# Performance work log

Hardware: AMD Instinct MI355X
Metric: run time of the kernel (lower is better)

## Reference

```python
import jax, jax.numpy as jnp
import numpy as np

# BinarizeConv2dSDP hyperparameters (from init_kwargs): SDP rank K and output scale.
SCALE = 1.0
K = 2
EPS = 1e-5  # BatchNorm2d default eps


@jax.custom_vjp
def binarize(x):
    # deterministic sign binarization (1-bit)
    return jnp.sign(x)

def _bin_fwd(x):
    return jnp.sign(x), x

def _bin_bwd(x, g):
    # straight-through estimator with hardtanh clipping, as in standard BNN training
    return (g * (jnp.abs(x) <= 1.0).astype(g.dtype),)

binarize.defvjp(_bin_fwd, _bin_bwd)


def conv3x3(x, w, stride=1):
    # x: [N, C, H, W], w: [O, I, 3, 3], padding=1
    return jax.lax.conv_general_dilated(
        x, w,
        window_strides=(stride, stride),
        padding=((1, 1), (1, 1)),
        dimension_numbers=("NCHW", "OIHW", "NCHW"),
    )


def binconv(x, w, stride=1):
    # binarized-input, binarized-weight conv with SDP scale
    return conv3x3(binarize(x), binarize(w), stride) * (SCALE / K)


def batchnorm(x, gamma, beta):
    # training-mode BatchNorm2d over (N, H, W)
    m = jnp.mean(x, axis=(0, 2, 3), keepdims=True)
    v = jnp.var(x, axis=(0, 2, 3), keepdims=True)
    xn = (x - m) * jax.lax.rsqrt(v + EPS)
    return xn * gamma[None, :, None, None] + beta[None, :, None, None]


def setup_inputs() -> dict:
    key = jax.random.key(0)
    k1, k2, k3 = jax.random.split(key, 3)
    N, C, H, W = 32, 256, 56, 56
    x = jax.random.normal(k1, (N, C, H, W), dtype=jnp.float32)
    w1 = jax.random.normal(k2, (C, C, 3, 3), dtype=jnp.float32) * 0.05
    w2 = jax.random.normal(k3, (C, C, 3, 3), dtype=jnp.float32) * 0.05
    g1 = jnp.ones((C,), jnp.float32)
    b1 = jnp.zeros((C,), jnp.float32)
    g2 = jnp.ones((C,), jnp.float32)
    b2 = jnp.zeros((C,), jnp.float32)
    return {"x": x, "w1": w1, "g1": g1, "b1": b1, "w2": w2, "g2": g2, "b2": b2}


def reference(x, w1, g1, b1, w2, g2, b2):
    # out = hardtanh(bn1(conv1(x)))
    out = jnp.clip(batchnorm(binconv(x, w1, 1), g1, b1), -1.0, 1.0)
    # out = bn2(conv2(out)) + shortcut(x)  (identity shortcut: stride=1, in_planes==planes)
    out = batchnorm(binconv(out, w2, 1), g2, b2) + x
    # final hardtanh
    return jnp.clip(out, -1.0, 1.0)
```

## Files before the change

kernel.cpp:

```cpp
#include <hip/hip_runtime.h>
#include <stdint.h>

#define NB    32
#define C     256
#define HH    56
#define WW    56
#define HW    3136
#define P_TOT 100352
#define PW    58
#define PHW   3364
#define NPAD  107648
#define EPSBN 1e-5f

__device__ __forceinline__ uint64_t shflx64(uint64_t v, int m) {
    int lo = __shfl_xor((int)(uint32_t)v, m, 64);
    int hi = __shfl_xor((int)(uint32_t)(v >> 32), m, 64);
    return ((uint64_t)(uint32_t)hi << 32) | (uint32_t)lo;
}
__device__ __forceinline__ uint64_t bt64(uint64_t M, int lane) {
    const uint64_t mk[6] = {0x5555555555555555ULL, 0x3333333333333333ULL,
                            0x0F0F0F0F0F0F0F0FULL, 0x00FF00FF00FF00FFULL,
                            0x0000FFFF0000FFFFULL, 0x00000000FFFFFFFFULL};
#pragma unroll
    for (int k = 0; k < 6; ++k) {
        int s = 1 << k;
        uint64_t mA = mk[k];
        uint64_t v = shflx64(M, s);
        M = (lane & s) ? ((M & ~mA) | ((v & ~mA) >> s))
                       : ((M &  mA) | ((v &  mA) << s));
    }
    return M;
}

__global__ __launch_bounds__(256) void pack_wgt(const float* __restrict__ w1,
                                                const float* __restrict__ w2,
                                                uint64_t* __restrict__ pw1,
                                                uint64_t* __restrict__ pw2,
                                                int* __restrict__ pc1,
                                                int* __restrict__ pc2) {
    int gw = blockIdx.x * 4 + (threadIdx.x >> 6);
    int lane = threadIdx.x & 63;
    int set = gw / 9216;
    int r = gw - set * 9216;
    int wd = r & 3, q = r >> 2;
    int t = q % 9, co = q / 9;
    const float* w = set ? w2 : w1;
    float v = w[(size_t)co * 2304 + (size_t)(wd * 64 + lane) * 9 + t];
    unsigned long long m = __ballot(v >= 0.0f);
    if (lane == 0) {
        uint64_t* pw = set ? pw2 : pw1;
        int* pc = set ? pc2 : pc1;
        pw[(size_t)(wd * 256 + co) * 10 + t] = m;
        pc[(co * 9 + t) * 4 + wd] = (int)__popcll(m);
    }
}

__global__ __launch_bounds__(256) void build_K(const int* __restrict__ pc1,
                                               const int* __restrict__ pc2,
                                               unsigned short* __restrict__ K1,
                                               unsigned short* __restrict__ K2) {
    int tid = blockIdx.x * 256 + threadIdx.x;
    int set = tid / 2304;
    int r = tid - set * 2304;
    int pat = r >> 8, co = r & 255;
    int pv = pat / 3, pq = pat - pv * 3;
    const int* pc = set ? pc2 : pc1;
    int k = 0, corr = 0;
#pragma unroll
    for (int t = 0; t < 9; ++t) {
        int ty = t / 3, tx = t - ty * 3;
        bool inv = (pv == 0 && ty == 0) || (pv == 2 && ty == 2) ||
                   (pq == 0 && tx == 0) || (pq == 2 && tx == 2);
        if (inv) {
            ++k;
            const int* p = pc + (co * 9 + t) * 4;
            corr += p[0] + p[1] + p[2] + p[3];
        }
    }
    unsigned short* K = set ? K2 : K1;
    K[pat * 256 + co] = (unsigned short)(256 * (9 - k) + 2 * corr);
}

__global__ __launch_bounds__(256) void zero_halo(uint64_t* __restrict__ px1,
                                                 uint64_t* __restrict__ px2) {
    int idx = blockIdx.x * 256 + threadIdx.x;
    if (idx >= NPAD) return;
    int pp = idx % PHW;
    int ph = pp / PW, pw_ = pp - ph * PW;
    if (ph == 0 || ph == PW - 1 || pw_ == 0 || pw_ == PW - 1) {
#pragma unroll
        for (int wd = 0; wd < 4; ++wd) {
            px1[(size_t)wd * NPAD + idx] = 0ull;
            px2[(size_t)wd * NPAD + idx] = 0ull;
        }
    }
}

__global__ __launch_bounds__(256) void pack_act(const float* __restrict__ x,
                                                uint64_t* __restrict__ px) {
    int wid = blockIdx.x * 4 + (threadIdx.x >> 6);
    int lane = threadIdx.x & 63;
    int wd = wid & 3;
    int g = wid >> 2;
    int n = g / 49, gi = g - n * 49;
    const float* xp = x + ((size_t)n * C + wd * 64) * HW + gi * 64 + lane;
    uint64_t M = 0;
#pragma unroll
    for (int c = 0; c < 64; ++c) {
        float v = xp[(size_t)c * HW];
        unsigned long long m = __ballot(v >= 0.0f);
        if (lane == c) M = m;
    }
    M = bt64(M, lane);
    int p = gi * 64 + lane;
    int h = p / WW, w = p - h * WW;
    px[(size_t)wd * NPAD + (size_t)n * PHW + (size_t)(h + 1) * PW + (w + 1)] = M;
}

__global__ __launch_bounds__(256, 3) void bconv(const uint64_t* __restrict__ px,
                                                const uint64_t* __restrict__ pw,
                                                const unsigned short* __restrict__ Kt,
                                                short* __restrict__ sout) {
    __shared__ uint64_t lw[2560];
    int co0 = blockIdx.y * 64;
#pragma unroll 1
    for (int i = threadIdx.x; i < 2560; i += 256) {
        int wd = i / 640, j = i - wd * 640;
        lw[i] = pw[(size_t)(wd * 256 + co0) * 10 + j];
    }
    __syncthreads();

    int p = blockIdx.x * 256 + threadIdx.x;
    int n = p / HW, rem = p - n * HW;
    int h = rem / WW, w = rem - h * WW;
    size_t pp = (size_t)n * PHW + (size_t)(h + 1) * PW + (w + 1);

    int acc[64];
#pragma unroll
    for (int c = 0; c < 64; ++c) acc[c] = 0;

#pragma unroll 1
    for (int wd = 0; wd < 4; ++wd) {
        const uint64_t* xb = px + (size_t)wd * NPAD + pp;
        uint64_t x0 = xb[-PW - 1], x1 = xb[-PW], x2 = xb[-PW + 1];
        uint64_t x3 = xb[-1],      x4 = xb[0],   x5 = xb[1];
        uint64_t x6 = xb[PW - 1],  x7 = xb[PW],  x8 = xb[PW + 1];
        const uint64_t* wb = lw + wd * 640;
#pragma unroll
        for (int c = 0; c < 64; ++c) {
            const uint64_t* wq = wb + c * 10;
            int r = acc[c];
            r += __popcll(x0 ^ wq[0]);
            r += __popcll(x1 ^ wq[1]);
            r += __popcll(x2 ^ wq[2]);
            r += __popcll(x3 ^ wq[3]);
            r += __popcll(x4 ^ wq[4]);
            r += __popcll(x5 ^ wq[5]);
            r += __popcll(x6 ^ wq[6]);
            r += __popcll(x7 ^ wq[7]);
            r += __popcll(x8 ^ wq[8]);
            acc[c] = r;
        }
    }

    int pv = (h == 0) ? 0 : ((h == HH - 1) ? 2 : 1);
    int pq = (w == 0) ? 0 : ((w == WW - 1) ? 2 : 1);
    const unsigned short* Kp = Kt + (pv * 3 + pq) * 256 + co0;
    short* op = sout + ((size_t)n * C + co0) * HW + rem;
#pragma unroll
    for (int c = 0; c < 64; ++c)
        op[(size_t)c * HW] = (short)((int)Kp[c] - 2 * acc[c]);
}

__global__ __launch_bounds__(256) void stats(const short* __restrict__ s,
                                             const float* __restrict__ g,
                                             const float* __restrict__ b,
                                             float* __restrict__ A,
                                             float* __restrict__ Bv) {
    int c = blockIdx.x;
    int sum = 0;
    long long sq = 0;
#pragma unroll 4
    for (int k = threadIdx.x; k < 12544; k += 256) {
        int n = k / 392, rr = k - n * 392;
        const int4* p = (const int4*)(s + ((size_t)n * C + c) * HW + rr * 8);
        int4 v = *p;
#pragma unroll
        for (int j = 0; j < 4; ++j) {
            int u = (&v.x)[j];
            int s0 = (int)(short)(u & 0xFFFF);
            int s1 = u >> 16;
            sum += s0 + s1;
            sq += (long long)(s0 * s0 + s1 * s1);
        }
    }
    long long lsum = sum;
#pragma unroll
    for (int off = 32; off; off >>= 1) {
        lsum += __shfl_down(lsum, off, 64);
        sq   += __shfl_down(sq,   off, 64);
    }
    __shared__ long long r0[4], r1[4];
    int lane = threadIdx.x & 63, wv = threadIdx.x >> 6;
    if (lane == 0) { r0[wv] = lsum; r1[wv] = sq; }
    __syncthreads();
    if (threadIdx.x == 0) {
        long long S = r0[0] + r0[1] + r0[2] + r0[3];
        long long Q = r1[0] + r1[1] + r1[2] + r1[3];
        float m  = 0.5f  * (float)S / (float)P_TOT;
        float e2 = 0.25f * (float)Q / (float)P_TOT;
        float var = e2 - m * m;
        float a = g[c] * rsqrtf(var + EPSBN);
        A[c]  = 0.5f * a;
        Bv[c] = b[c] - m * a;
    }
}

__global__ __launch_bounds__(256) void bnpack(const short* __restrict__ s,
                                              const float* __restrict__ A,
                                              const float* __restrict__ Bv,
                                              uint64_t* __restrict__ px) {
    __shared__ float sA[256], sB[256];
    sA[threadIdx.x] = A[threadIdx.x];
    sB[threadIdx.x] = Bv[threadIdx.x];
    __syncthreads();
    int wid = blockIdx.x * 4 + (threadIdx.x >> 6);
    int lane = threadIdx.x & 63;
    int wd = wid & 3;
    int g = wid >> 2;
    int n = g / 49, gi = g - n * 49;
    const short* sp = s + ((size_t)n * C + wd * 64) * HW + gi * 64 + lane;
    uint64_t M = 0;
#pragma unroll
    for (int c = 0; c < 64; ++c) {
        float y = (float)sp[(size_t)c * HW] * sA[wd * 64 + c] + sB[wd * 64 + c];
        unsigned long long m = __ballot(y >= 0.0f);
        if (lane == c) M = m;
    }
    M = bt64(M, lane);
    int p = gi * 64 + lane;
    int h = p / WW, w = p - h * WW;
    px[(size_t)wd * NPAD + (size_t)n * PHW + (size_t)(h + 1) * PW + (w + 1)] = M;
}

__global__ __launch_bounds__(256) void finalize(const short* __restrict__ s,
                                                const float* __restrict__ x,
                                                const float* __restrict__ A,
                                                const float* __restrict__ Bv,
                                                float* __restrict__ out) {
    int i = blockIdx.x * 256 + threadIdx.x;
    int c = (i / 784) & 255;
    short4 sv = ((const short4*)s)[i];
    float4 xv = ((const float4*)x)[i];
    float a = A[c], bb = Bv[c];
    float4 o;
    o.x = fminf(1.0f, fmaxf(-1.0f, (float)sv.x * a + bb + xv.x));
    o.y = fminf(1.0f, fmaxf(-1.0f, (float)sv.y * a + bb + xv.y));
    o.z = fminf(1.0f, fmaxf(-1.0f, (float)sv.z * a + bb + xv.z));
    o.w = fminf(1.0f, fmaxf(-1.0f, (float)sv.w * a + bb + xv.w));
    ((float4*)out)[i] = o;
}

extern "C" void kernel_launch(void* const* d_in, const int* in_sizes, int n_in,
                              void* d_out, int out_size, void* d_ws, size_t ws_size,
                              hipStream_t stream) {
    const float* x  = (const float*)d_in[0];
    const float* w1 = (const float*)d_in[1];
    const float* g1 = (const float*)d_in[2];
    const float* b1 = (const float*)d_in[3];
    const float* w2 = (const float*)d_in[4];
    const float* g2 = (const float*)d_in[5];
    const float* b2 = (const float*)d_in[6];
    float* out = (float*)d_out;

    char* ws = (char*)d_ws;
    uint64_t* pw1 = (uint64_t*)ws;          ws += 4 * 256 * 10 * 8;
    uint64_t* pw2 = (uint64_t*)ws;          ws += 4 * 256 * 10 * 8;
    int* pc1 = (int*)ws;                    ws += 9216 * 4;
    int* pc2 = (int*)ws;                    ws += 9216 * 4;
    unsigned short* K1 = (unsigned short*)ws; ws += 8192;
    unsigned short* K2 = (unsigned short*)ws; ws += 8192;
    float* A1 = (float*)ws;                 ws += 1024;
    float* B1 = (float*)ws;                 ws += 1024;
    float* A2 = (float*)ws;                 ws += 1024;
    float* B2 = (float*)ws;                 ws += 1024;
    uint64_t* px1 = (uint64_t*)ws;          ws += (size_t)4 * NPAD * 8;
    uint64_t* px2 = (uint64_t*)ws;          ws += (size_t)4 * NPAD * 8;
    short* s16 = (short*)ws;

    zero_halo<<<(NPAD + 255) / 256, 256, 0, stream>>>(px1, px2);
    pack_wgt<<<4608, 256, 0, stream>>>(w1, w2, pw1, pw2, pc1, pc2);
    build_K<<<18, 256, 0, stream>>>(pc1, pc2, K1, K2);
    pack_act<<<1568, 256, 0, stream>>>(x, px1);

    bconv<<<dim3(P_TOT / 256, 4), 256, 0, stream>>>(px1, pw1, K1, s16);
    stats<<<C, 256, 0, stream>>>(s16, g1, b1, A1, B1);
    bnpack<<<1568, 256, 0, stream>>>(s16, A1, B1, px2);

    bconv<<<dim3(P_TOT / 256, 4), 256, 0, stream>>>(px2, pw2, K2, s16);
    stats<<<C, 256, 0, stream>>>(s16, g2, b2, A2, B2);

    finalize<<<(P_TOT * C / 4) / 256, 256, 0, stream>>>(s16, x, A2, B2, out);
}
```

Baseline: 566.4 us.

## Restructure binary conv to register-resident activations and channel-major scratch layout

```diff
diff --git a/kernel.cpp b/kernel.cpp
--- a/kernel.cpp
+++ b/kernel.cpp
@@ -11,6 +11,9 @@
 #define PHW   3364
 #define NPAD  107648
 #define EPSBN 1e-5f
+
+#define KEEP9(a) asm volatile("" :: "v"(a[0]), "v"(a[1]), "v"(a[2]), "v"(a[3]), \
+    "v"(a[4]), "v"(a[5]), "v"(a[6]), "v"(a[7]), "v"(a[8]))
 
 __device__ __forceinline__ uint64_t shflx64(uint64_t v, int m) {
     int lo = __shfl_xor((int)(uint32_t)v, m, 64);
@@ -50,7 +53,7 @@
     if (lane == 0) {
         uint64_t* pw = set ? pw2 : pw1;
         int* pc = set ? pc2 : pc1;
-        pw[(size_t)(wd * 256 + co) * 10 + t] = m;
+        pw[(size_t)co * 40 + wd * 9 + t] = m;
         pc[(co * 9 + t) * 4 + wd] = (int)__popcll(m);
     }
 }
@@ -81,23 +84,24 @@
     K[pat * 256 + co] = (unsigned short)(256 * (9 - k) + 2 * corr);
 }
 
-__global__ __launch_bounds__(256) void zero_halo(uint64_t* __restrict__ px1,
-                                                 uint64_t* __restrict__ px2) {
-    int idx = blockIdx.x * 256 + threadIdx.x;
-    if (idx >= NPAD) return;
-    int pp = idx % PHW;
-    int ph = pp / PW, pw_ = pp - ph * PW;
-    if (ph == 0 || ph == PW - 1 || pw_ == 0 || pw_ == PW - 1) {
-#pragma unroll
-        for (int wd = 0; wd < 4; ++wd) {
-            px1[(size_t)wd * NPAD + idx] = 0ull;
-            px2[(size_t)wd * NPAD + idx] = 0ull;
-        }
-    }
-}
-
 __global__ __launch_bounds__(256) void pack_act(const float* __restrict__ x,
-                                                uint64_t* __restrict__ px) {
+                                                uint64_t* __restrict__ px1,
+                                                uint64_t* __restrict__ px2) {
+    if (blockIdx.x >= 1568) {
+        int u = (blockIdx.x - 1568) * 256 + threadIdx.x;
+        if (u >= 29184) return;
+        int wd = u & 3, v = u >> 2;
+        int n = v / 228, cell = v - n * 228;
+        int ph, pw_;
+        if (cell < 58)       { ph = 0;          pw_ = cell; }
+        else if (cell < 116) { ph = 57;         pw_ = cell - 58; }
+        else if (cell < 172) { ph = cell - 115; pw_ = 0; }
+        else                 { ph = cell - 171; pw_ = 57; }
+        size_t idx = (size_t)wd * NPAD + (size_t)n * PHW + (size_t)ph * PW + pw_;
+        px1[idx] = 0ull;
+        px2[idx] = 0ull;
+        return;
+    }
     int wid = blockIdx.x * 4 + (threadIdx.x >> 6);
     int lane = threadIdx.x & 63;
     int wd = wid & 3;
@@ -114,95 +118,87 @@
     M = bt64(M, lane);
     int p = gi * 64 + lane;
     int h = p / WW, w = p - h * WW;
-    px[(size_t)wd * NPAD + (size_t)n * PHW + (size_t)(h + 1) * PW + (w + 1)] = M;
-}
-
-__global__ __launch_bounds__(256, 3) void bconv(const uint64_t* __restrict__ px,
-                                                const uint64_t* __restrict__ pw,
+    px1[(size_t)wd * NPAD + (size_t)n * PHW + (size_t)(h + 1) * PW + (w + 1)] = M;
+}
+
+__global__ __launch_bounds__(256, 2) void bconv(const uint64_t* __restrict__ px,
+                                                const uint64_t* __restrict__ pwt,
                                                 const unsigned short* __restrict__ Kt,
                                                 short* __restrict__ sout) {
-    __shared__ uint64_t lw[2560];
-    int co0 = blockIdx.y * 64;
+    __shared__ unsigned short Kl[2304];
 #pragma unroll 1
-    for (int i = threadIdx.x; i < 2560; i += 256) {
-        int wd = i / 640, j = i - wd * 640;
-        lw[i] = pw[(size_t)(wd * 256 + co0) * 10 + j];
-    }
-    __syncthreads();
+    for (int i = threadIdx.x; i < 2304; i += 256) Kl[i] = Kt[i];
 
     int p = blockIdx.x * 256 + threadIdx.x;
     int n = p / HW, rem = p - n * HW;
     int h = rem / WW, w = rem - h * WW;
-    size_t pp = (size_t)n * PHW + (size_t)(h + 1) * PW + (w + 1);
-
-    int acc[64];
-#pragma unroll
-    for (int c = 0; c < 64; ++c) acc[c] = 0;
-
-#pragma unroll 1
+    size_t base = (size_t)n * PHW + (size_t)(h + 1) * PW + (w + 1);
+
+    uint64_t xt[36];
+#pragma unroll
     for (int wd = 0; wd < 4; ++wd) {
-        const uint64_t* xb = px + (size_t)wd * NPAD + pp;
-        uint64_t x0 = xb[-PW - 1], x1 = xb[-PW], x2 = xb[-PW + 1];
-        uint64_t x3 = xb[-1],      x4 = xb[0],   x5 = xb[1];
-        uint64_t x6 = xb[PW - 1],  x7 = xb[PW],  x8 = xb[PW + 1];
-        const uint64_t* wb = lw + wd * 640;
-#pragma unroll
-        for (int c = 0; c < 64; ++c) {
-            const uint64_t* wq = wb + c * 10;
-            int r = acc[c];
-            r += __popcll(x0 ^ wq[0]);
-            r += __popcll(x1 ^ wq[1]);
-            r += __popcll(x2 ^ wq[2]);
-            r += __popcll(x3 ^ wq[3]);
-            r += __popcll(x4 ^ wq[4]);
-            r += __popcll(x5 ^ wq[5]);
-            r += __popcll(x6 ^ wq[6]);
-            r += __popcll(x7 ^ wq[7]);
-            r += __popcll(x8 ^ wq[8]);
-            acc[c] = r;
-        }
-    }
+        const uint64_t* xb = px + (size_t)wd * NPAD + base;
+        xt[wd * 9 + 0] = xb[-PW - 1]; xt[wd * 9 + 1] = xb[-PW]; xt[wd * 9 + 2] = xb[-PW + 1];
+        xt[wd * 9 + 3] = xb[-1];      xt[wd * 9 + 4] = xb[0];   xt[wd * 9 + 5] = xb[1];
+        xt[wd * 9 + 6] = xb[PW - 1];  xt[wd * 9 + 7] = xb[PW];  xt[wd * 9 + 8] = xb[PW + 1];
+    }
+    __syncthreads();
 
     int pv = (h == 0) ? 0 : ((h == HH - 1) ? 2 : 1);
     int pq = (w == 0) ? 0 : ((w == WW - 1) ? 2 : 1);
-    const unsigned short* Kp = Kt + (pv * 3 + pq) * 256 + co0;
-    short* op = sout + ((size_t)n * C + co0) * HW + rem;
-#pragma unroll
-    for (int c = 0; c < 64; ++c)
-        op[(size_t)c * HW] = (short)((int)Kp[c] - 2 * acc[c]);
-}
-
-__global__ __launch_bounds__(256) void stats(const short* __restrict__ s,
-                                             const float* __restrict__ g,
-                                             const float* __restrict__ b,
-                                             float* __restrict__ A,
-                                             float* __restrict__ Bv) {
+    const unsigned short* Krow = Kl + ((pv * 3 + pq) << 8);
+
+    int co0 = blockIdx.y * 64;
+    short* op = sout + (size_t)co0 * P_TOT + p;
+#pragma unroll 2
+    for (int c = 0; c < 64; ++c) {
+        const uint64_t* wq = pwt + (size_t)(co0 + c) * 40;
+        KEEP9((xt + 0)); KEEP9((xt + 9)); KEEP9((xt + 18)); KEEP9((xt + 27));
+        int a0 = 0, a1 = 0, a2 = 0, a3 = 0;
+#pragma unroll
+        for (int t = 0; t < 9; ++t) {
+            a0 += __popcll(xt[t]      ^ wq[t]);
+            a1 += __popcll(xt[9 + t]  ^ wq[9 + t]);
+            a2 += __popcll(xt[18 + t] ^ wq[18 + t]);
+            a3 += __popcll(xt[27 + t] ^ wq[27 + t]);
+        }
+        int dot = (int)Krow[co0 + c] - 2 * (a0 + a1 + a2 + a3);
+        op[(size_t)c * P_TOT] = (short)dot;
+    }
+}
+
+__global__ __launch_bounds__(256) void statsAB(const short* __restrict__ s,
+                                               const float* __restrict__ g,
+                                               const float* __restrict__ b,
+                                               float* __restrict__ A,
+                                               float* __restrict__ Bv) {
     int c = blockIdx.x;
+    const int4* sp = (const int4*)(s + (size_t)c * P_TOT);
     int sum = 0;
-    long long sq = 0;
+    long long sqq = 0;
 #pragma unroll 4
-    for (int k = threadIdx.x; k < 12544; k += 256) {
-        int n = k / 392, rr = k - n * 392;
-        const int4* p = (const int4*)(s + ((size_t)n * C + c) * HW + rr * 8);
-        int4 v = *p;
+    for (int i = threadIdx.x; i < 12544; i += 256) {
+        int4 v = sp[i];
+        int sq8 = 0;
 #pragma unroll
         for (int j = 0; j < 4; ++j) {
             int u = (&v.x)[j];
             int s0 = (int)(short)(u & 0xFFFF);
             int s1 = u >> 16;
             sum += s0 + s1;
-            sq += (long long)(s0 * s0 + s1 * s1);
+            sq8 += s0 * s0 + s1 * s1;
         }
+        sqq += sq8;
     }
     long long lsum = sum;
 #pragma unroll
     for (int off = 32; off; off >>= 1) {
         lsum += __shfl_down(lsum, off, 64);
-        sq   += __shfl_down(sq,   off, 64);
+        sqq  += __shfl_down(sqq,  off, 64);
     }
     __shared__ long long r0[4], r1[4];
     int lane = threadIdx.x & 63, wv = threadIdx.x >> 6;
-    if (lane == 0) { r0[wv] = lsum; r1[wv] = sq; }
+    if (lane == 0) { r0[wv] = lsum; r1[wv] = sqq; }
     __syncthreads();
     if (threadIdx.x == 0) {
         long long S = r0[0] + r0[1] + r0[2] + r0[3];
@@ -220,26 +216,22 @@
                                               const float* __restrict__ A,
                                               const float* __restrict__ Bv,
                                               uint64_t* __restrict__ px) {
-    __shared__ float sA[256], sB[256];
-    sA[threadIdx.x] = A[threadIdx.x];
-    sB[threadIdx.x] = Bv[threadIdx.x];
-    __syncthreads();
     int wid = blockIdx.x * 4 + (threadIdx.x >> 6);
     int lane = threadIdx.x & 63;
     int wd = wid & 3;
     int g = wid >> 2;
-    int n = g / 49, gi = g - n * 49;
-    const short* sp = s + ((size_t)n * C + wd * 64) * HW + gi * 64 + lane;
+    const short* sp = s + (size_t)(wd * 64) * P_TOT + g * 64 + lane;
     uint64_t M = 0;
 #pragma unroll
     for (int c = 0; c < 64; ++c) {
-        float y = (float)sp[(size_t)c * HW] * sA[wd * 64 + c] + sB[wd * 64 + c];
+        float y = (float)sp[(size_t)c * P_TOT] * A[wd * 64 + c] + Bv[wd * 64 + c];
         unsigned long long m = __ballot(y >= 0.0f);
         if (lane == c) M = m;
     }
     M = bt64(M, lane);
-    int p = gi * 64 + lane;
-    int h = p / WW, w = p - h * WW;
+    int p = g * 64 + lane;
+    int n = p / HW, rem = p - n * HW;
+    int h = rem / WW, w = rem - h * WW;
     px[(size_t)wd * NPAD + (size_t)n * PHW + (size_t)(h + 1) * PW + (w + 1)] = M;
 }
 
@@ -249,16 +241,19 @@
                                                 const float* __restrict__ Bv,
                                                 float* __restrict__ out) {
     int i = blockIdx.x * 256 + threadIdx.x;
-    int c = (i / 784) & 255;
+    int c = i / 25088;
+    int r4 = i - c * 25088;
+    int n = r4 / 784, hw4 = r4 - n * 784;
     short4 sv = ((const short4*)s)[i];
-    float4 xv = ((const float4*)x)[i];
+    size_t gx = (size_t)(n * C + c) * 784 + hw4;
+    float4 xv = ((const float4*)x)[gx];
     float a = A[c], bb = Bv[c];
     float4 o;
     o.x = fminf(1.0f, fmaxf(-1.0f, (float)sv.x * a + bb + xv.x));
     o.y = fminf(1.0f, fmaxf(-1.0f, (float)sv.y * a + bb + xv.y));
     o.z = fminf(1.0f, fmaxf(-1.0f, (float)sv.z * a + bb + xv.z));
     o.w = fminf(1.0f, fmaxf(-1.0f, (float)sv.w * a + bb + xv.w));
-    ((float4*)out)[i] = o;
+    ((float4*)out)[gx] = o;
 }
 
 extern "C" void kernel_launch(void* const* d_in, const int* in_sizes, int n_in,
@@ -274,31 +269,30 @@
     float* out = (float*)d_out;
 
     char* ws = (char*)d_ws;
-    uint64_t* pw1 = (uint64_t*)ws;          ws += 4 * 256 * 10 * 8;
-    uint64_t* pw2 = (uint64_t*)ws;          ws += 4 * 256 * 10 * 8;
-    int* pc1 = (int*)ws;                    ws += 9216 * 4;
-    int* pc2 = (int*)ws;                    ws += 9216 * 4;
+    uint64_t* pwt1 = (uint64_t*)ws;           ws += 256 * 40 * 8;
+    uint64_t* pwt2 = (uint64_t*)ws;           ws += 256 * 40 * 8;
+    int* pc1 = (int*)ws;                      ws += 9216 * 4;
+    int* pc2 = (int*)ws;                      ws += 9216 * 4;
     unsigned short* K1 = (unsigned short*)ws; ws += 8192;
     unsigned short* K2 = (unsigned short*)ws; ws += 8192;
-    float* A1 = (float*)ws;                 ws += 1024;
-    float* B1 = (float*)ws;                 ws += 1024;
-    float* A2 = (float*)ws;                 ws += 1024;
-    float* B2 = (float*)ws;                 ws += 1024;
-    uint64_t* px1 = (uint64_t*)ws;          ws += (size_t)4 * NPAD * 8;
-    uint64_t* px2 = (uint64_t*)ws;          ws += (size_t)4 * NPAD * 8;
+    float* A1 = (float*)ws;                   ws += 1024;
+    float* B1 = (float*)ws;                   ws += 1024;
+    float* A2 = (float*)ws;                   ws += 1024;
+    float* B2 = (float*)ws;                   ws += 1024;
+    uint64_t* px1 = (uint64_t*)ws;            ws += (size_t)4 * NPAD * 8;
+    uint64_t* px2 = (uint64_t*)ws;            ws += (size_t)4 * NPAD * 8;
     short* s16 = (short*)ws;
 
-    zero_halo<<<(NPAD + 255) / 256, 256, 0, stream>>>(px1, px2);
-    pack_wgt<<<4608, 256, 0, stream>>>(w1, w2, pw1, pw2, pc1, pc2);
+    pack_wgt<<<4608, 256, 0, stream>>>(w1, w2, pwt1, pwt2, pc1, pc2);
     build_K<<<18, 256, 0, stream>>>(pc1, pc2, K1, K2);
-    pack_act<<<1568, 256, 0, stream>>>(x, px1);
-
-    bconv<<<dim3(P_TOT / 256, 4), 256, 0, stream>>>(px1, pw1, K1, s16);
-    stats<<<C, 256, 0, stream>>>(s16, g1, b1, A1, B1);
+    pack_act<<<1568 + 114, 256, 0, stream>>>(x, px1, px2);
+
+    bconv<<<dim3(392, 4), 256, 0, stream>>>(px1, pwt1, K1, s16);
+    statsAB<<<C, 256, 0, stream>>>(s16, g1, b1, A1, B1);
     bnpack<<<1568, 256, 0, stream>>>(s16, A1, B1, px2);
 
-    bconv<<<dim3(P_TOT / 256, 4), 256, 0, stream>>>(px2, pw2, K2, s16);
-    stats<<<C, 256, 0, stream>>>(s16, g2, b2, A2, B2);
+    bconv<<<dim3(392, 4), 256, 0, stream>>>(px2, pwt2, K2, s16);
+    statsAB<<<C, 256, 0, stream>>>(s16, g2, b2, A2, B2);
 
     finalize<<<(P_TOT * C / 4) / 256, 256, 0, stream>>>(s16, x, A2, B2, out);
 }
```

New measurement: 559.3 us. About the same (-1.3%).
